# Optimization experiments

Measured on AMD Instinct MI355X. Metric: run time of the kernel, lower is better.

The kernel has to match this reference:

```python
import jax, jax.numpy as jnp
import numpy as np

B, T, IN, H, L = 64, 512, 512, 512, 2


def setup_inputs() -> dict:
    key = jax.random.key(0)
    ks = jax.random.split(key, 7)
    s_ih = 1.0 / np.sqrt(H)
    x = jax.random.normal(ks[0], (B, T, IN), dtype=jnp.float32)
    encoder_h = jax.random.normal(ks[1], (L, B, H), dtype=jnp.float32)
    # stacked GRUCell params per layer (input_size == hidden_size so stackable)
    W_ih = jax.random.uniform(ks[2], (L, 3 * H, IN), jnp.float32, -s_ih, s_ih)
    W_hh = jax.random.uniform(ks[3], (L, 3 * H, H), jnp.float32, -s_ih, s_ih)
    b_ih = jax.random.uniform(ks[4], (L, 3 * H), jnp.float32, -s_ih, s_ih)
    b_hh = jax.random.uniform(ks[5], (L, 3 * H), jnp.float32, -s_ih, s_ih)
    return {"x": x, "encoder_h": encoder_h, "W_ih": W_ih, "W_hh": W_hh,
            "b_ih": b_ih, "b_hh": b_hh}


def _gru_cell(x, h, W_ih, W_hh, b_ih, b_hh):
    # torch.nn.GRUCell math
    gi = x @ W_ih.T + b_ih            # [B, 3H]
    gh = h @ W_hh.T + b_hh            # [B, 3H]
    i_r, i_z, i_n = jnp.split(gi, 3, axis=-1)
    h_r, h_z, h_n = jnp.split(gh, 3, axis=-1)
    r = jax.nn.sigmoid(i_r + h_r)
    z = jax.nn.sigmoid(i_z + h_z)
    n = jnp.tanh(i_n + r * h_n)
    return (1.0 - z) * n + z * h


def reference(x, encoder_h, W_ih, W_hh, b_ih, b_hh):
    num_layers = W_ih.shape[0]

    def step(h_carry, x_t):
        hs = []
        inp = x_t
        for j in range(num_layers):  # small static layer loop
            h_new = _gru_cell(inp, h_carry[j], W_ih[j], W_hh[j], b_ih[j], b_hh[j])
            hs.append(h_new)
            inp = h_new
        return tuple(hs), inp

    h0 = tuple(encoder_h[j] for j in range(num_layers))
    xs = jnp.swapaxes(x, 0, 1)                 # [T, B, IN]
    h_final, outs = jax.lax.scan(step, h0, xs)  # outs: [T, B, H]
    out = jnp.swapaxes(outs, 0, 1)             # [B, T, H]
    h = jnp.stack(h_final, axis=0)             # [L, B, H]
    return out, h
```

## Files before the change

kernel.cpp:

```cpp
#include <hip/hip_runtime.h>


#define NBLK 256
#define NTHR 512
#define Bsz  64
#define Tlen 512
#define Kd   512
#define Hd   512
#define KC   64
#define LP   67

__device__ __forceinline__ float sigf(float v){ return 1.0f/(1.0f+__expf(-v)); }
__device__ __forceinline__ float tanhx(float v){
  float e=__expf(-2.0f*fabsf(v)); float t=(1.0f-e)/(1.0f+e); return v<0.0f?-t:t;
}
__device__ __forceinline__ unsigned umin2(unsigned a, unsigned b){ return a<b?a:b; }

__device__ __forceinline__ void st_coh(float* p, float v){
  asm volatile("global_store_dword %0, %1, off sc0 sc1" :: "v"(p), "v"(v) : "memory");
}
__device__ __forceinline__ void st_coh_u(unsigned* p, unsigned v){
  asm volatile("global_store_dword %0, %1, off sc0 sc1" :: "v"(p), "v"(v) : "memory");
}
__device__ __forceinline__ void wait_vm0(){ asm volatile("s_waitcnt vmcnt(0)" ::: "memory"); }

__device__ __forceinline__ void grid_barrier(unsigned* slots, unsigned target, int tid){
  wait_vm0();
  __syncthreads();
  if(tid == 0) st_coh_u(slots + blockIdx.x, target);
  if(tid < 64){
    const unsigned* p0 = slots + tid;
    for(;;){
      unsigned a,b,c,d;
      asm volatile(
        "global_load_dword %0, %4, off sc0 sc1\n\t"
        "global_load_dword %1, %5, off sc0 sc1\n\t"
        "global_load_dword %2, %6, off sc0 sc1\n\t"
        "global_load_dword %3, %7, off sc0 sc1\n\t"
        "s_waitcnt vmcnt(0)"
        : "=v"(a),"=v"(b),"=v"(c),"=v"(d)
        : "v"(p0), "v"(p0+64), "v"(p0+128), "v"(p0+192)
        : "memory");
      unsigned m = umin2(umin2(a,b), umin2(c,d));
      #pragma unroll
      for(int off=32; off; off>>=1)
        m = umin2(m, (unsigned)__shfl_xor((int)m, off, 64));
      if(m >= target) break;
      __builtin_amdgcn_s_sleep(1);
    }
  }
  __syncthreads();
  __builtin_amdgcn_fence(__ATOMIC_ACQUIRE, "agent");
}

__device__ __forceinline__ void stageA(float* sbuf, const float* __restrict__ x,
                                       int t, int ch, int tid){
  #pragma unroll
  for(int it=0; it<2; ++it){
    int q  = it*NTHR + tid;
    int b  = q >> 4;
    int k4 = (q & 15) << 2;
    const float4 v = *(const float4*)(x + ((size_t)b*Tlen + t)*Kd + ch*KC + k4);
    sbuf[(k4+0)*LP + b] = v.x;
    sbuf[(k4+1)*LP + b] = v.y;
    sbuf[(k4+2)*LP + b] = v.z;
    sbuf[(k4+3)*LP + b] = v.w;
  }
}

extern "C" __global__ void __launch_bounds__(NTHR, 2)
gru_persist(const float* __restrict__ x,
            const float* __restrict__ eh,
            const float* __restrict__ Wih,
            const float* __restrict__ Whh,
            const float* __restrict__ bih,
            const float* __restrict__ bhh,
            float* __restrict__ out,
            float* __restrict__ ws)
{
  __shared__ float smem[2*KC*LP];

  unsigned* slots = (unsigned*)ws;
  float* h0T = ws + 256;
  float* h1T = h0T + 2*Kd*Bsz;
  float* htail = out + (size_t)Bsz*Tlen*Hd;

  const int tid  = threadIdx.x;
  const int lane = tid & 63;
  const int wv   = __builtin_amdgcn_readfirstlane(tid >> 6);
  const int cell = blockIdx.x >> 7;
  const int cb   = blockIdx.x & 127;
  const int col0 = cb * 4;
  unsigned bar = 1;

  {
    int i = blockIdx.x*NTHR + tid;
    if(i < 2*Kd*Bsz){
      int l = i >> 15, k = (i >> 6) & 511, b = i & 63;
      float v = eh[(size_t)(l*Bsz + b)*Hd + k];
      st_coh((l ? h1T : h0T) + Kd*Bsz + k*Bsz + b, v);
    }
  }
  grid_barrier(slots, bar, tid); bar++;

  const float* WiB = Wih + (size_t)cell*3*Hd*Kd + (size_t)col0*Kd;
  const float* WhB = Whh + (size_t)cell*3*Hd*Kd + (size_t)col0*Kd;
  const int ec = wv & 3;
  const int ecol = col0 + ec;
  const float bi0 = bih[cell*1536 + 0*Hd + ecol] + bhh[cell*1536 + 0*Hd + ecol];
  const float bi1 = bih[cell*1536 + 1*Hd + ecol] + bhh[cell*1536 + 1*Hd + ecol];
  const float bi2 = bih[cell*1536 + 2*Hd + ecol];
  const float bh2 = bhh[cell*1536 + 2*Hd + ecol];

  for(int t = 0; t <= Tlen; ++t){
    const bool active = (cell == 0) ? (t < Tlen) : (t >= 1);
    if(active){
      const int s = (cell == 0) ? t : (t - 1);
      float* hbase = (cell == 0) ? h0T : h1T;
      const float* hprev = hbase + ((s+1)&1)*Kd*Bsz;
      float*       hout  = hbase + (s&1)*Kd*Bsz;
      const float* inT   = h0T + (s&1)*Kd*Bsz;

      float pr[4]={0,0,0,0}, pz[4]={0,0,0,0}, pni[4]={0,0,0,0}, pnh[4]={0,0,0,0};

      if(cell == 0){
        stageA(smem, x, t, 0, tid);
        __syncthreads();
        for(int ch = 0; ch < 8; ++ch){
          const float* cur = smem + (ch&1)*(KC*LP);
          if(ch < 7) stageA(smem + ((ch+1)&1)*(KC*LP), x, t, ch+1, tid);
          #pragma unroll
          for(int j = 0; j < 8; ++j){
            const int kl = (wv<<3) + j;
            const int kg = (ch<<6) + kl;
            const float xv = cur[kl*LP + lane];
            const float hv = hprev[kg*Bsz + lane];
            #pragma unroll
            for(int c = 0; c < 4; ++c){
              pr[c]  = fmaf(xv, WiB[(size_t)c*Kd + kg], pr[c]);
              pz[c]  = fmaf(xv, WiB[(size_t)Hd*Kd + c*Kd + kg], pz[c]);
              pni[c] = fmaf(xv, WiB[(size_t)2*Hd*Kd + c*Kd + kg], pni[c]);
              pr[c]  = fmaf(hv, WhB[(size_t)c*Kd + kg], pr[c]);
              pz[c]  = fmaf(hv, WhB[(size_t)Hd*Kd + c*Kd + kg], pz[c]);
              pnh[c] = fmaf(hv, WhB[(size_t)2*Hd*Kd + c*Kd + kg], pnh[c]);
            }
          }
          __syncthreads();
        }
      } else {
        #pragma unroll 8
        for(int j = 0; j < 64; ++j){
          const int kg = (wv<<6) + j;
          const float xv = inT[kg*Bsz + lane];
          const float hv = hprev[kg*Bsz + lane];
          #pragma unroll
          for(int c = 0; c < 4; ++c){
            pr[c]  = fmaf(xv, WiB[(size_t)c*Kd + kg], pr[c]);
            pz[c]  = fmaf(xv, WiB[(size_t)Hd*Kd + c*Kd + kg], pz[c]);
            pni[c] = fmaf(xv, WiB[(size_t)2*Hd*Kd + c*Kd + kg], pni[c]);
            pr[c]  = fmaf(hv, WhB[(size_t)c*Kd + kg], pr[c]);
            pz[c]  = fmaf(hv, WhB[(size_t)Hd*Kd + c*Kd + kg], pz[c]);
            pnh[c] = fmaf(hv, WhB[(size_t)2*Hd*Kd + c*Kd + kg], pnh[c]);
          }
        }
        __syncthreads();
      }

      float* red = smem;
      #pragma unroll
      for(int c = 0; c < 4; ++c){
        red[(((c<<2)+0)*8 + wv)*64 + lane] = pr[c];
        red[(((c<<2)+1)*8 + wv)*64 + lane] = pz[c];
        red[(((c<<2)+2)*8 + wv)*64 + lane] = pni[c];
        red[(((c<<2)+3)*8 + wv)*64 + lane] = pnh[c];
      }
      __syncthreads();
      if(wv < 4){
        const int c = wv;
        float spr=0.f, spz=0.f, spni=0.f, spnh=0.f;
        #pragma unroll
        for(int w = 0; w < 8; ++w){
          spr  += red[(((c<<2)+0)*8 + w)*64 + lane];
          spz  += red[(((c<<2)+1)*8 + w)*64 + lane];
          spni += red[(((c<<2)+2)*8 + w)*64 + lane];
          spnh += red[(((c<<2)+3)*8 + w)*64 + lane];
        }
        const int col = col0 + c;
        const float hkeep = hprev[col*Bsz + lane];
        const float r = sigf(spr + bi0);
        const float z = sigf(spz + bi1);
        const float n = tanhx(spni + bi2 + r*(spnh + bh2));
        const float hnew = (1.0f - z)*n + z*hkeep;
        st_coh(hout + col*Bsz + lane, hnew);
        if(cell == 1)
          out[((size_t)lane*Tlen + s)*Hd + col] = hnew;
      }
    }
    grid_barrier(slots, bar, tid); bar++;
  }

  {
    int i = blockIdx.x*NTHR + tid;
    if(i < 2*Kd*Bsz){
      int l = i >> 15, b = (i >> 9) & 63, c = i & 511;
      const float* src = (l ? h1T : h0T) + Kd*Bsz;
      htail[i] = src[c*Bsz + b];
    }
  }
}

extern "C" void kernel_launch(void* const* d_in, const int* in_sizes, int n_in,
                              void* d_out, int out_size, void* d_ws, size_t ws_size,
                              hipStream_t stream) {
  (void)in_sizes; (void)n_in; (void)out_size; (void)ws_size;
  const float* x   = (const float*)d_in[0];
  const float* eh  = (const float*)d_in[1];
  const float* Wih = (const float*)d_in[2];
  const float* Whh = (const float*)d_in[3];
  const float* bih = (const float*)d_in[4];
  const float* bhh = (const float*)d_in[5];
  float* out = (float*)d_out;
  float* ws  = (float*)d_ws;

  hipMemsetAsync(d_ws, 0, 1024, stream);

  void* args[] = {(void*)&x, (void*)&eh, (void*)&Wih, (void*)&Whh,
                  (void*)&bih, (void*)&bhh, (void*)&out, (void*)&ws};
  hipLaunchCooperativeKernel((const void*)gru_persist, dim3(NBLK), dim3(NTHR),
                             args, 0, stream);
}
```

Measured before the change: 19.83 ms.

## Cache per-block GRU weight slices in LDS and prefetch hidden-state operands

```diff
diff --git a/kernel.cpp b/kernel.cpp
--- a/kernel.cpp
+++ b/kernel.cpp
@@ -68,6 +68,28 @@
   }
 }
 
+__device__ __forceinline__ void gru_fma(const float* __restrict__ wlds, int kg,
+                                        const float* xv, const float* hv,
+                                        float* pr, float* pz, float* pni, float* pnh)
+{
+  float4 w[24];
+  #pragma unroll
+  for(int s = 0; s < 24; ++s)
+    w[s] = *(const float4*)(wlds + s*Kd + kg);
+  #pragma unroll
+  for(int u = 0; u < 4; ++u){
+    #pragma unroll
+    for(int c = 0; c < 4; ++c){
+      pr[c]  = fmaf(xv[u], (&w[     c].x)[u], pr[c]);
+      pz[c]  = fmaf(xv[u], (&w[ 4 + c].x)[u], pz[c]);
+      pni[c] = fmaf(xv[u], (&w[ 8 + c].x)[u], pni[c]);
+      pr[c]  = fmaf(hv[u], (&w[12 + c].x)[u], pr[c]);
+      pz[c]  = fmaf(hv[u], (&w[16 + c].x)[u], pz[c]);
+      pnh[c] = fmaf(hv[u], (&w[20 + c].x)[u], pnh[c]);
+    }
+  }
+}
+
 extern "C" __global__ void __launch_bounds__(NTHR, 2)
 gru_persist(const float* __restrict__ x,
             const float* __restrict__ eh,
@@ -79,6 +101,7 @@
             float* __restrict__ ws)
 {
   __shared__ float smem[2*KC*LP];
+  __shared__ float wlds[24*Kd];
 
   unsigned* slots = (unsigned*)ws;
   float* h0T = ws + 256;
@@ -94,6 +117,21 @@
   unsigned bar = 1;
 
   {
+    const float* WiC = Wih + (size_t)cell*3*Hd*Kd;
+    const float* WhC = Whh + (size_t)cell*3*Hd*Kd;
+    #pragma unroll 1
+    for(int i = tid; i < 24*(Kd/4); i += NTHR){
+      const int s   = i >> 7;
+      const int k4  = (i & 127) << 2;
+      const int mat = (s >= 12);
+      const int r   = s - 12*mat;
+      const int g   = r >> 2, c = r & 3;
+      const float* src = (mat ? WhC : WiC) + ((size_t)(g*Hd + col0 + c))*Kd + k4;
+      *(float4*)(wlds + (size_t)s*Kd + k4) = *(const float4*)src;
+    }
+  }
+
+  {
     int i = blockIdx.x*NTHR + tid;
     if(i < 2*Kd*Bsz){
       int l = i >> 15, k = (i >> 6) & 511, b = i & 63;
@@ -103,8 +141,6 @@
   }
   grid_barrier(slots, bar, tid); bar++;
 
-  const float* WiB = Wih + (size_t)cell*3*Hd*Kd + (size_t)col0*Kd;
-  const float* WhB = Whh + (size_t)cell*3*Hd*Kd + (size_t)col0*Kd;
   const int ec = wv & 3;
   const int ecol = col0 + ec;
   const float bi0 = bih[cell*1536 + 0*Hd + ecol] + bhh[cell*1536 + 0*Hd + ecol];
@@ -130,39 +166,40 @@
           const float* cur = smem + (ch&1)*(KC*LP);
           if(ch < 7) stageA(smem + ((ch+1)&1)*(KC*LP), x, t, ch+1, tid);
           #pragma unroll
-          for(int j = 0; j < 8; ++j){
-            const int kl = (wv<<3) + j;
+          for(int jj = 0; jj < 8; jj += 4){
+            const int kl = (wv<<3) + jj;
             const int kg = (ch<<6) + kl;
-            const float xv = cur[kl*LP + lane];
-            const float hv = hprev[kg*Bsz + lane];
+            float xv[4], hv[4];
             #pragma unroll
-            for(int c = 0; c < 4; ++c){
-              pr[c]  = fmaf(xv, WiB[(size_t)c*Kd + kg], pr[c]);
-              pz[c]  = fmaf(xv, WiB[(size_t)Hd*Kd + c*Kd + kg], pz[c]);
-              pni[c] = fmaf(xv, WiB[(size_t)2*Hd*Kd + c*Kd + kg], pni[c]);
-              pr[c]  = fmaf(hv, WhB[(size_t)c*Kd + kg], pr[c]);
-              pz[c]  = fmaf(hv, WhB[(size_t)Hd*Kd + c*Kd + kg], pz[c]);
-              pnh[c] = fmaf(hv, WhB[(size_t)2*Hd*Kd + c*Kd + kg], pnh[c]);
+            for(int u = 0; u < 4; ++u){
+              xv[u] = cur[(kl+u)*LP + lane];
+              hv[u] = hprev[(kg+u)*Bsz + lane];
             }
+            gru_fma(wlds, kg, xv, hv, pr, pz, pni, pnh);
           }
           __syncthreads();
         }
       } else {
-        #pragma unroll 8
-        for(int j = 0; j < 64; ++j){
-          const int kg = (wv<<6) + j;
-          const float xv = inT[kg*Bsz + lane];
-          const float hv = hprev[kg*Bsz + lane];
+        const int kg0 = (wv<<6);
+        float xv[4], hv[4], xn[4], hn[4];
+        #pragma unroll
+        for(int u = 0; u < 4; ++u){
+          xv[u] = inT[(kg0+u)*Bsz + lane];
+          hv[u] = hprev[(kg0+u)*Bsz + lane];
+        }
+        #pragma unroll 1
+        for(int j4 = 0; j4 < 60; j4 += 4){
+          const int kg = kg0 + j4;
           #pragma unroll
-          for(int c = 0; c < 4; ++c){
-            pr[c]  = fmaf(xv, WiB[(size_t)c*Kd + kg], pr[c]);
-            pz[c]  = fmaf(xv, WiB[(size_t)Hd*Kd + c*Kd + kg], pz[c]);
-            pni[c] = fmaf(xv, WiB[(size_t)2*Hd*Kd + c*Kd + kg], pni[c]);
-            pr[c]  = fmaf(hv, WhB[(size_t)c*Kd + kg], pr[c]);
-            pz[c]  = fmaf(hv, WhB[(size_t)Hd*Kd + c*Kd + kg], pz[c]);
-            pnh[c] = fmaf(hv, WhB[(size_t)2*Hd*Kd + c*Kd + kg], pnh[c]);
+          for(int u = 0; u < 4; ++u){
+            xn[u] = inT[(kg+4+u)*Bsz + lane];
+            hn[u] = hprev[(kg+4+u)*Bsz + lane];
           }
-        }
+          gru_fma(wlds, kg, xv, hv, pr, pz, pni, pnh);
+          #pragma unroll
+          for(int u = 0; u < 4; ++u){ xv[u] = xn[u]; hv[u] = hn[u]; }
+        }
+        gru_fma(wlds, kg0 + 60, xv, hv, pr, pz, pni, pnh);
         __syncthreads();
       }
 
```

New measurement: 19.72 ms. About the same (-0.6%).
